# Kernel optimization log

Hardware: AMD Instinct MI355X
Metric: run time of the kernel (lower is better)

## Reference

```python
import jax, jax.numpy as jnp
import numpy as np


def setup_inputs() -> dict:
    key = jax.random.key(0)
    k1, k2, k3, k4 = jax.random.split(key, 4)
    B, D, F = 524288, 64, 32
    stdv = 1.0 / np.sqrt(D)
    x = jax.random.normal(k1, (B, D), dtype=jnp.float32)
    us = jax.random.uniform(k2, (F, D), dtype=jnp.float32, minval=-stdv, maxval=stdv)
    ws = jax.random.uniform(k3, (F, D), dtype=jnp.float32, minval=-stdv, maxval=stdv)
    bs = jax.random.uniform(k4, (F,), dtype=jnp.float32, minval=-0.01, maxval=0.01)
    return {"x": x, "us": us, "ws": ws, "bs": bs}


def _planar_step(carry, params):
    z, sum_log_det = carry
    u, w, b = params  # u,w: [D], b: scalar
    # constrained u for invertibility: u_hat = u + (softplus(wu) - 1 - wu) * w / ||w||
    wu = jnp.dot(u, w)
    u_hat = u + (jax.nn.softplus(wu) - 1.0 - wu) * w / jnp.linalg.norm(w)
    lin = z @ w + b                      # [B]
    h = jnp.tanh(lin)                    # [B]
    z_new = z + u_hat[None, :] * h[:, None]
    h_prime = 1.0 - h * h                # [B]
    # psi @ u_hat = h'(lin) * (w . u_hat)
    log_det = jnp.log(jnp.abs(1.0 + h_prime * jnp.dot(w, u_hat)))
    return (z_new, sum_log_det + log_det), None


def reference(x, us, ws, bs):
    init = (x, jnp.zeros(x.shape[0], dtype=x.dtype))
    (z, sum_log_det), _ = jax.lax.scan(_planar_step, init, (us, ws, bs))
    return z, sum_log_det
```

## Files before the change

kernel.cpp:

```cpp
#include <hip/hip_runtime.h>
#include <math.h>


#define NF_D 64
#define NF_F 32

typedef float f4 __attribute__((ext_vector_type(4)));
typedef float f32x4v __attribute__((ext_vector_type(4)));
typedef unsigned int u32;
typedef u32 u32x4 __attribute__((ext_vector_type(4)));
typedef short bf16x8 __attribute__((ext_vector_type(8)));

#define WS_WF   0
#define WS_UF   2048
#define WS_GT   3072
#define WS_WUH  4096
#define WS_TOT  4128

__device__ __forceinline__ u32 fbits(float x){ union{float f;u32 u;} c; c.f=x; return c.u; }
__device__ __forceinline__ float asf(u32 u){ union{u32 u;float f;} c; c.u=u; return c.f; }
__device__ __forceinline__ u32 bfrnd(float x){ u32 b=fbits(x); return (b + 0x7FFFu + ((b>>16)&1u)) >> 16; }
__device__ __forceinline__ bf16x8 asbf(u32x4 v){ union{u32x4 u; bf16x8 b;} c; c.u=v; return c.b; }

__global__ void nf_precompute(const float* __restrict__ us,
                              const float* __restrict__ ws,
                              u32* __restrict__ wsb) {
  __shared__ float s_u[NF_F][NF_D];
  float* wsf = (float*)wsb;
  int t = threadIdx.x;
  if (t < NF_F) {
    const float* u = us + t * NF_D;
    const float* w = ws + t * NF_D;
    float wu = 0.f, n2 = 0.f;
    for (int d = 0; d < NF_D; ++d) {
      wu = fmaf(u[d], w[d], wu);
      n2 = fmaf(w[d], w[d], n2);
    }
    float sp = fmaxf(wu, 0.f) + log1pf(expf(-fabsf(wu)));
    float coef = (sp - 1.f - wu) / sqrtf(n2);
    for (int d = 0; d < NF_D; ++d)
      s_u[t][d] = fmaf(coef, w[d], u[d]);
    wsf[WS_WUH + t] = fmaf(coef, n2, wu);
  }
  __syncthreads();
  for (int idx = t; idx < 8 * 64; idx += 256) {
    int lin = idx >> 6, l = idx & 63;
    int Mt = lin >> 2, Kt = (lin >> 1) & 1, p = lin & 1;
    int fm = 16 * Mt + (l & 15);
    int kb = 32 * Kt + 8 * (l >> 4);
    for (int i = 0; i < 4; ++i) {
      u32 pr[2];
      for (int e = 0; e < 2; ++e) {
        float w = ws[fm * NF_D + kb + 2 * i + e];
        u32 hb = fbits(w) & 0xFFFF0000u;
        pr[e] = (p == 0) ? (hb >> 16) : (fbits(w - asf(hb)) >> 16);
      }
      wsb[WS_WF + (lin * 64 + l) * 4 + i] = pr[0] | (pr[1] << 16);
    }
  }
  for (int idx = t; idx < 4 * 64; idx += 256) {
    int l = idx & 63;
    int d = 16 * (idx >> 6) + (l & 15);
    int fb = 8 * (l >> 4);
    for (int i = 0; i < 4; ++i) {
      u32 r0 = bfrnd(s_u[fb + 2 * i][d]);
      u32 r1 = bfrnd(s_u[fb + 2 * i + 1][d]);
      wsb[WS_UF + idx * 4 + i] = r0 | (r1 << 16);
    }
  }
  for (int i = t; i < NF_F * NF_F; i += 256) {
    int f = i >> 5, g = i & 31;
    float s = 0.f;
    if (g < f) {
      const float* w = ws + f * NF_D;
      for (int d = 0; d < NF_D; ++d) s = fmaf(s_u[g][d], w[d], s);
    }
    wsf[WS_GT + i] = s;
  }
}

__device__ __forceinline__ float fast_tanh(float x) {
  float e = __builtin_amdgcn_exp2f(x * 2.885390081777927f);
  return 1.f - 2.f * __builtin_amdgcn_rcpf(e + 1.f);
}

#define MFMA __builtin_amdgcn_mfma_f32_16x16x32_bf16

__global__ __launch_bounds__(256) void nf_main(
    const float* __restrict__ x,
    const float* __restrict__ bs,
    const u32* __restrict__ wsb,
    float* __restrict__ out_z,
    float* __restrict__ out_ld,
    int B) {
  __shared__ float S[4][2048];
  const float* wsf = (const float*)wsb;

  int wave = threadIdx.x >> 6;
  int l = threadIdx.x & 63;
  int ntiles = B / 64;
  int tile = blockIdx.x * 4 + wave;
  if (tile >= ntiles) tile = ntiles - 1;
  float* Sw = S[wave];

  bf16x8 Wf[2][2][2], Uf[4];
  #pragma unroll
  for (int q = 0; q < 8; ++q)
    Wf[q >> 2][(q >> 1) & 1][q & 1] =
        asbf(*(const u32x4*)(wsb + WS_WF + (q * 64 + l) * 4));
  #pragma unroll
  for (int Nt = 0; Nt < 4; ++Nt)
    Uf[Nt] = asbf(*(const u32x4*)(wsb + WS_UF + (Nt * 64 + l) * 4));

  const float* xt = x + (size_t)tile * 64 * NF_D;

  #pragma unroll
  for (int Nt = 0; Nt < 4; ++Nt) {
    bf16x8 Xh[2], Xl[2];
    #pragma unroll
    for (int Kt = 0; Kt < 2; ++Kt) {
      const f4* xp = (const f4*)(xt + ((l & 15) + 16 * Nt) * NF_D +
                                 32 * Kt + 8 * (l >> 4));
      f4 xa = xp[0], xb = xp[1];
      float xs[8] = {xa.x, xa.y, xa.z, xa.w, xb.x, xb.y, xb.z, xb.w};
      u32x4 hw, lw;
      #pragma unroll
      for (int i = 0; i < 4; ++i) {
        u32 b0 = fbits(xs[2 * i]), b1 = fbits(xs[2 * i + 1]);
        u32 h0 = b0 & 0xFFFF0000u, h1 = b1 & 0xFFFF0000u;
        hw[i] = (h0 >> 16) | h1;
        lw[i] = (fbits(xs[2 * i] - asf(h0)) >> 16) |
                (fbits(xs[2 * i + 1] - asf(h1)) & 0xFFFF0000u);
      }
      Xh[Kt] = asbf(hw);
      Xl[Kt] = asbf(lw);
    }
    #pragma unroll
    for (int Mt = 0; Mt < 2; ++Mt) {
      f32x4v a = {0.f, 0.f, 0.f, 0.f};
      #pragma unroll
      for (int Kt = 0; Kt < 2; ++Kt) {
        a = MFMA(Wf[Mt][Kt][0], Xh[Kt], a, 0, 0, 0);
        a = MFMA(Wf[Mt][Kt][0], Xl[Kt], a, 0, 0, 0);
        a = MFMA(Wf[Mt][Kt][1], Xh[Kt], a, 0, 0, 0);
      }
      int b = (l & 15) + 16 * Nt;
      int fc = 16 * Mt + 4 * (l >> 4);
      #pragma unroll
      for (int r = 0; r < 4; ++r)
        Sw[b * 32 + ((fc + r) ^ (b & 31))] = a[r];
    }
  }

  const float* gt = wsf + WS_GT;
  const float* wuhp = wsf + WS_WUH;
  f4 hq[8];
  #pragma unroll
  for (int q = 0; q < 8; ++q) hq[q] = (f4)(0.f);
  float ldp = 1.f;
  #pragma unroll
  for (int f = 0; f < NF_F; ++f) {
    const f4* g4 = (const f4*)(gt + f * 32);
    f4 a = (f4)(0.f);
    #pragma unroll
    for (int q = 0; q < (f + 3) / 4; ++q)
      a += g4[q] * hq[q];
    float s = Sw[l * 32 + (f ^ (l & 31))] + bs[f] +
              ((a.x + a.y) + (a.z + a.w));
    float hf = fast_tanh(s);
    ldp *= fmaf(fmaf(-hf, hf, 1.f), wuhp[f], 1.f);
    hq[f >> 2][f & 3] = hf;
  }
  #pragma unroll
  for (int i = 0; i < 16; ++i) {
    u32 pk = (fbits(hq[i >> 1][(i & 1) * 2]) >> 16) |
             (fbits(hq[i >> 1][(i & 1) * 2 + 1]) & 0xFFFF0000u);
    Sw[i * 64 + l] = asf(pk);
  }

  bf16x8 Hf[4];
  #pragma unroll
  for (int Nt = 0; Nt < 4; ++Nt) {
    u32x4 hw;
    #pragma unroll
    for (int i = 0; i < 4; ++i)
      hw[i] = fbits(Sw[(4 * (l >> 4) + i) * 64 + (l & 15) + 16 * Nt]);
    Hf[Nt] = asbf(hw);
  }

  float* zt = out_z + (size_t)tile * 64 * NF_D;
  #pragma unroll
  for (int Ntb = 0; Ntb < 4; ++Ntb) {
    #pragma unroll
    for (int Mtd = 0; Mtd < 4; ++Mtd) {
      f32x4v zz = {0.f, 0.f, 0.f, 0.f};
      zz = MFMA(Uf[Mtd], Hf[Ntb], zz, 0, 0, 0);
      int b = (l & 15) + 16 * Ntb;
      int d0 = 16 * Mtd + 4 * (l >> 4);
      f4 xr = *(const f4*)(xt + b * NF_D + d0);
      f4 zv = {zz[0] + xr.x, zz[1] + xr.y, zz[2] + xr.z, zz[3] + xr.w};
      *(f4*)(zt + b * NF_D + d0) = zv;
    }
  }
  out_ld[(size_t)tile * 64 + l] =
      __builtin_amdgcn_logf(fabsf(ldp)) * 0.6931471805599453f;
}

extern "C" void kernel_launch(void* const* d_in, const int* in_sizes, int n_in,
                              void* d_out, int out_size, void* d_ws, size_t ws_size,
                              hipStream_t stream) {
  const float* x    = (const float*)d_in[0];
  const float* us   = (const float*)d_in[1];
  const float* ws_p = (const float*)d_in[2];
  const float* bs   = (const float*)d_in[3];
  const int B = in_sizes[0] / NF_D;

  u32* wsbuf = (u32*)d_ws;
  float* out = (float*)d_out;

  nf_precompute<<<1, 256, 0, stream>>>(us, ws_p, wsbuf);
  const int ntiles = B / 64;
  const int grid = (ntiles + 3) / 4;
  nf_main<<<grid, 256, 0, stream>>>(x, bs, wsbuf, out,
                                    out + (size_t)B * NF_D, B);
}
```

Measured before the change: 85.87 us.

## Use one-wave blocks and vectorized LDS staging of pre-activations

Switches nf_main from four-wave blocks to single-wave 64-thread blocks, one tile per block, with an 8 KB LDS buffer. Projection results are now written and read back as float4 with a swizzle on 16-byte chunks. All 32 pre-activations plus biases are loaded into registers up front, and that same register array is overwritten with the tanh outputs, so the serial flow loop no longer does a per-step LDS read and bias load. The aim is cheaper LDS traffic and finer-grained scheduling, at the cost of more workgroups and possibly higher register pressure.

```diff
diff --git a/kernel.cpp b/kernel.cpp
--- a/kernel.cpp
+++ b/kernel.cpp
@@ -86,22 +86,19 @@
 
 #define MFMA __builtin_amdgcn_mfma_f32_16x16x32_bf16
 
-__global__ __launch_bounds__(256) void nf_main(
+__global__ __launch_bounds__(64) void nf_main(
     const float* __restrict__ x,
     const float* __restrict__ bs,
     const u32* __restrict__ wsb,
     float* __restrict__ out_z,
     float* __restrict__ out_ld,
     int B) {
-  __shared__ float S[4][2048];
+  __shared__ float Sw[2048];
   const float* wsf = (const float*)wsb;
 
-  int wave = threadIdx.x >> 6;
-  int l = threadIdx.x & 63;
-  int ntiles = B / 64;
-  int tile = blockIdx.x * 4 + wave;
-  if (tile >= ntiles) tile = ntiles - 1;
-  float* Sw = S[wave];
+  int l = threadIdx.x;
+  int tile = blockIdx.x;
+  float* Sp = Sw;
 
   bf16x8 Wf[2][2][2], Uf[4];
   #pragma unroll
@@ -145,18 +142,20 @@
         a = MFMA(Wf[Mt][Kt][1], Xh[Kt], a, 0, 0, 0);
       }
       int b = (l & 15) + 16 * Nt;
-      int fc = 16 * Mt + 4 * (l >> 4);
-      #pragma unroll
-      for (int r = 0; r < 4; ++r)
-        Sw[b * 32 + ((fc + r) ^ (b & 31))] = a[r];
+      int qw = 4 * Mt + (l >> 4);
+      f4 av = {a[0], a[1], a[2], a[3]};
+      *(f4*)(Sp + b * 32 + 4 * (qw ^ (b & 7))) = av;
     }
   }
 
   const float* gt = wsf + WS_GT;
   const float* wuhp = wsf + WS_WUH;
-  f4 hq[8];
-  #pragma unroll
-  for (int q = 0; q < 8; ++q) hq[q] = (f4)(0.f);
+  const f4* bs4 = (const f4*)bs;
+  f4 st[8];
+  #pragma unroll
+  for (int q = 0; q < 8; ++q)
+    st[q] = *(const f4*)(Sp + l * 32 + 4 * (q ^ (l & 7))) + bs4[q];
+
   float ldp = 1.f;
   #pragma unroll
   for (int f = 0; f < NF_F; ++f) {
@@ -164,18 +163,17 @@
     f4 a = (f4)(0.f);
     #pragma unroll
     for (int q = 0; q < (f + 3) / 4; ++q)
-      a += g4[q] * hq[q];
-    float s = Sw[l * 32 + (f ^ (l & 31))] + bs[f] +
-              ((a.x + a.y) + (a.z + a.w));
+      a += g4[q] * st[q];
+    float s = st[f >> 2][f & 3] + ((a.x + a.y) + (a.z + a.w));
     float hf = fast_tanh(s);
     ldp *= fmaf(fmaf(-hf, hf, 1.f), wuhp[f], 1.f);
-    hq[f >> 2][f & 3] = hf;
+    st[f >> 2][f & 3] = hf;
   }
   #pragma unroll
   for (int i = 0; i < 16; ++i) {
-    u32 pk = (fbits(hq[i >> 1][(i & 1) * 2]) >> 16) |
-             (fbits(hq[i >> 1][(i & 1) * 2 + 1]) & 0xFFFF0000u);
-    Sw[i * 64 + l] = asf(pk);
+    u32 pk = (fbits(st[i >> 1][(i & 1) * 2]) >> 16) |
+             (fbits(st[i >> 1][(i & 1) * 2 + 1]) & 0xFFFF0000u);
+    Sp[i * 64 + l] = asf(pk);
   }
 
   bf16x8 Hf[4];
@@ -184,7 +182,7 @@
     u32x4 hw;
     #pragma unroll
     for (int i = 0; i < 4; ++i)
-      hw[i] = fbits(Sw[(4 * (l >> 4) + i) * 64 + (l & 15) + 16 * Nt]);
+      hw[i] = fbits(Sp[(4 * (l >> 4) + i) * 64 + (l & 15) + 16 * Nt]);
     Hf[Nt] = asbf(hw);
   }
 
@@ -220,7 +218,6 @@
 
   nf_precompute<<<1, 256, 0, stream>>>(us, ws_p, wsbuf);
   const int ntiles = B / 64;
-  const int grid = (ntiles + 3) / 4;
-  nf_main<<<grid, 256, 0, stream>>>(x, bs, wsbuf, out,
-                                    out + (size_t)B * NF_D, B);
-}
+  nf_main<<<ntiles, 64, 0, stream>>>(x, bs, wsbuf, out,
+                                     out + (size_t)B * NF_D, B);
+}
```

After: 90.02 us. +4.8%, slower.
